# Performance work log

Measured on AMD Instinct MI355X. Metric: run time of the kernel, lower is better.

The kernel has to match this reference:

```python
import jax, jax.numpy as jnp
import numpy as np

H = 16      # num_heads
HD = 128    # head_dim = embed_dim // num_heads
BS = 64     # NSA block_size
SEL = 8     # selected blocks per query (block_counts)
WIN = 64    # sliding window (left) size
BASE = 10000.0


def _rope(t):
    # t: [b, n, h, hd]; rotary LRPE (lrpe_type=1)
    n, hd = t.shape[1], t.shape[-1]
    half = hd // 2
    inv = 1.0 / (BASE ** (jnp.arange(half, dtype=jnp.float32) / half))
    th = jnp.arange(n, dtype=jnp.float32)[:, None] * inv[None, :]  # [n, half]
    cos = jnp.cos(th)[None, :, None, :]
    sin = jnp.sin(th)[None, :, None, :]
    t1, t2 = t[..., :half], t[..., half:]
    return jnp.concatenate([t1 * cos - t2 * sin, t1 * sin + t2 * cos], axis=-1)


def _nsa_forward(x, Wq, Wk, Wv, Wg, Wo):
    b, n, d = x.shape
    nb = n // BS
    scale = HD ** -0.5
    q = (x @ Wq).reshape(b, n, H, HD)
    k = (x @ Wk).reshape(b, n, H, HD)
    v = (x @ Wv).reshape(b, n, H, HD)
    g = jax.nn.sigmoid(x @ Wg)                   # [b, n, 3H]
    g_cmp, g_slc, g_swa = jnp.split(g, 3, axis=-1)
    q = _rope(q)
    k = _rope(k)
    idx = jnp.arange(n)

    # --- compression branch: mean-pooled KV blocks, causal over fully-past blocks
    k_cmp = k.reshape(b, nb, BS, H, HD).mean(axis=2)   # [b, nb, h, hd]
    v_cmp = v.reshape(b, nb, BS, H, HD).mean(axis=2)
    s_cmp = jnp.einsum('bnhd,bmhd->bhnm', q, k_cmp) * scale  # [b, h, n, nb]
    blk_end = (jnp.arange(nb) + 1) * BS - 1
    cmp_mask = idx[:, None] >= blk_end[None, :]        # [n, nb]
    p_cmp = jax.nn.softmax(jnp.where(cmp_mask[None, None], s_cmp, -1e30), axis=-1)
    p_cmp = p_cmp * cmp_mask.any(-1)[None, None, :, None]  # zero rows with no valid block
    o_cmp = jnp.einsum('bhnm,bmhd->bnhd', p_cmp, v_cmp)

    # --- selection branch: top-k blocks by compressed scores, current block forced
    cur_blk = jax.nn.one_hot(idx // BS, nb, dtype=jnp.float32)  # [n, nb]
    imp = p_cmp + 2.0 * cur_blk[None, None]
    sel = jax.lax.top_k(imp, SEL)[1]                   # [b, h, n, SEL]
    blk_sel = jax.nn.one_hot(sel, nb).sum(-2) > 0      # [b, h, n, nb]
    causal = idx[:, None] >= idx[None, :]              # [n, n]
    slc_mask = blk_sel[..., idx // BS] & causal[None, None]  # [b, h, n, n]
    s_full = jnp.einsum('bnhd,bmhd->bhnm', q, k) * scale     # [b, h, n, n]
    p_slc = jax.nn.softmax(jnp.where(slc_mask, s_full, -1e30), axis=-1)
    o_slc = jnp.einsum('bhnm,bmhd->bnhd', p_slc, v)

    swa_mask = causal & (idx[:, None] - idx[None, :] <= WIN)
    p_swa = jax.nn.softmax(jnp.where(swa_mask[None, None], s_full, -1e30), axis=-1)
    o_swa = jnp.einsum('bhnm,bmhd->bnhd', p_swa, v)

    o = (o_cmp * g_cmp[..., None] + o_slc * g_slc[..., None]
         + o_swa * g_swa[..., None])                   # [b, n, h, hd]
    return o.reshape(b, n, H * HD) @ Wo


def setup_inputs() -> dict:
    key = jax.random.key(0)
    ks = jax.random.split(key, 6)
    B, N, D = 2, 1024, 2048
    std = 0.02
    return {
        'x': jax.random.normal(ks[0], (B, N, D), jnp.float32),
        'Wq': jax.random.normal(ks[1], (D, H * HD), jnp.float32) * std,
        'Wk': jax.random.normal(ks[2], (D, H * HD), jnp.float32) * std,
        'Wv': jax.random.normal(ks[3], (D, H * HD), jnp.float32) * std,
        'Wg': jax.random.normal(ks[4], (D, 3 * H), jnp.float32) * std,
        'Wo': jax.random.normal(ks[5], (H * HD, D), jnp.float32) * std,
    }


def reference(x, Wq, Wk, Wv, Wg, Wo):
    return _nsa_forward(x, Wq, Wk, Wv, Wg, Wo)
```

## Files before the change

kernel.cpp:

```cpp
#include <hip/hip_runtime.h>
#include <hip/hip_bf16.h>

#define HN   16
#define HDIM 128
#define NSEQ 1024
#define NBLK 16
#define BSZ  64
#define SCALE 0.08838834764831845f
#define QKV_STR 6400
#define KOFS 2048
#define VOFS 4096
#define GOFS 6144

typedef __attribute__((ext_vector_type(8))) short bfrag;
typedef __attribute__((ext_vector_type(4))) float facc;

__device__ __forceinline__ float bf2f(short s) {
  union { unsigned u; float f; } cv;
  cv.u = ((unsigned)(unsigned short)s) << 16;
  return cv.f;
}
__device__ __forceinline__ short f2bf(float f) {
  unsigned u = __float_as_uint(f);
  u = (u + 0x7fff + ((u >> 16) & 1)) >> 16;
  return (short)u;
}

#define ASYNC16(gp, lp)                                                    \
  __builtin_amdgcn_global_load_lds(                                        \
      (const __attribute__((address_space(1))) void*)(gp),                 \
      (__attribute__((address_space(3))) void*)(lp), 16, 0, 0)

#define MFMA16(a, b, c) __builtin_amdgcn_mfma_f32_16x16x32_bf16(a, b, c, 0, 0, 0)

__global__ __launch_bounds__(256) void prep(const float* __restrict__ Wq,
                                            const float* __restrict__ Wk,
                                            const float* __restrict__ Wv,
                                            const float* __restrict__ Wg,
                                            const float* __restrict__ x,
                                            short* __restrict__ w_t,
                                            short* __restrict__ x_bf,
                                            float2* __restrict__ tbl) {
  __shared__ float tile[32][33];
  const int z = blockIdx.z;
  const int bx = blockIdx.x * 32, by = blockIdx.y * 32;
  const int tx = threadIdx.x & 31, ty = threadIdx.x >> 5;
  if (z == 5) {
    if (blockIdx.y >= 4) return;
    int i = (blockIdx.y * 64 + blockIdx.x) * 256 + threadIdx.x;
    int d = i & 63, n = i >> 6;
    float inv = expf(-(float)d * (9.210340371976184f / 64.0f));
    float sn, cs;
    sincosf((float)n * inv, &sn, &cs);
    tbl[i] = make_float2(cs, sn);
    return;
  }
  if (z == 4) {
#pragma unroll
    for (int i = 0; i < 4; ++i) {
      const int row = by + ty + 8 * i;
      x_bf[(size_t)row * 2048 + bx + tx] = f2bf(x[(size_t)row * 2048 + bx + tx]);
    }
    return;
  }
  if (z == 3) {
    if (blockIdx.x >= 4) return;
#pragma unroll
    for (int i = 0; i < 4; ++i) {
      const int c = bx + tx;
      tile[ty + 8 * i][tx] = (c < 48) ? Wg[(size_t)(by + ty + 8 * i) * 48 + c] : 0.f;
    }
    __syncthreads();
#pragma unroll
    for (int i = 0; i < 4; ++i)
      w_t[(size_t)(GOFS + bx + ty + 8 * i) * 2048 + by + tx] = f2bf(tile[tx][ty + 8 * i]);
    return;
  }
  const float* src = (z == 0) ? Wq : (z == 1) ? Wk : Wv;
#pragma unroll
  for (int i = 0; i < 4; ++i)
    tile[ty + 8 * i][tx] = src[(size_t)(by + ty + 8 * i) * 2048 + bx + tx];
  __syncthreads();
#pragma unroll
  for (int i = 0; i < 4; ++i)
    w_t[(size_t)(z * 2048 + bx + ty + 8 * i) * 2048 + by + tx] = f2bf(tile[tx][ty + 8 * i]);
}

__global__ __launch_bounds__(256) void transpose_cast(const float* __restrict__ src,
                                                      short* __restrict__ dst) {
  __shared__ float tile[32][33];
  const int bx = blockIdx.x * 32, by = blockIdx.y * 32;
  const int tx = threadIdx.x & 31, ty = threadIdx.x >> 5;
#pragma unroll
  for (int i = 0; i < 4; ++i)
    tile[ty + 8 * i][tx] = src[(size_t)(by + ty + 8 * i) * 2048 + bx + tx];
  __syncthreads();
#pragma unroll
  for (int i = 0; i < 4; ++i)
    dst[(size_t)(bx + ty + 8 * i) * 2048 + by + tx] = f2bf(tile[tx][ty + 8 * i]);
}

__global__ __launch_bounds__(512, 1) void gemm256(const short* __restrict__ A,
                                                  const short* __restrict__ Bt,
                                                  short* __restrict__ C,
                                                  int M, int N, int K) {
  __shared__ short lds[2][2][16384];
  const int t = threadIdx.x;
  const int l = t & 63, w = t >> 6;
  const int wm = w >> 2, wn = w & 3;
  const int lm = l & 15, hi = l >> 4;
  const int lanexor = (lm & 7) << 3;
  const int kk0 = (hi * 8) ^ lanexor;
  const int L = blockIdx.x;
  const int item = (L & 7) * (gridDim.x >> 3) + (L >> 3);
  const int nrow = M >> 8;
  const int row0 = (item % nrow) * 256, col0 = (item / nrow) * 256;
  const int nt = K >> 6;

  const int srow = t >> 3;
  const int scol = 8 * ((t & 7) ^ (srow & 7));
  const short* Ab = A + (size_t)(row0 + srow) * K + scol;
  const short* Bb = Bt + (size_t)(col0 + srow) * K + scol;

#define STAGE(mat, srcbase, h, tau, buf)                                     \
  {                                                                          \
    const short* g_ = (srcbase) + (size_t)(h) * 128 * K + (size_t)(tau) * 64;\
    short* d_ = &lds[buf][mat][(h) * 8192 + t * 8];                          \
    ASYNC16(g_, d_);                                                         \
    ASYNC16(g_ + (size_t)64 * K, d_ + 4096);                                 \
  }

  facc acc[8][4] = {};
  bfrag af[8], bf0[4], bf1[4];

  STAGE(0, Ab, 0, 0, 0); STAGE(0, Ab, 1, 0, 0);
  STAGE(1, Bb, 0, 0, 0); STAGE(1, Bb, 1, 0, 0);
  STAGE(1, Bb, 0, 1, 1); STAGE(1, Bb, 1, 1, 1);
  asm volatile("s_waitcnt vmcnt(4)" ::: "memory");
  __builtin_amdgcn_s_barrier();

  for (int tau = 0; tau < nt; ++tau) {
    const int c = tau & 1;
    const int tA = (tau + 1 < nt) ? tau + 1 : nt - 1;
    const int tB = (tau + 2 < nt) ? tau + 2 : nt - 1;

#define DS_A(qm)                                                             \
  _Pragma("unroll") for (int ii = 0; ii < 4; ++ii) {                         \
    const int row_ = wm * 128 + (qm) * 64 + ii * 16 + lm;                    \
    af[ii * 2 + 0] = *(const bfrag*)&lds[c][0][row_ * 64 + kk0];             \
    af[ii * 2 + 1] = *(const bfrag*)&lds[c][0][row_ * 64 + (kk0 ^ 32)];      \
  }
#define DS_B(qn, arr)                                                        \
  _Pragma("unroll") for (int jj = 0; jj < 2; ++jj) {                         \
    const int row_ = wn * 64 + (qn) * 32 + jj * 16 + lm;                     \
    arr[jj * 2 + 0] = *(const bfrag*)&lds[c][1][row_ * 64 + kk0];            \
    arr[jj * 2 + 1] = *(const bfrag*)&lds[c][1][row_ * 64 + (kk0 ^ 32)];     \
  }
#define QUAD(qm, qn, arr)                                                    \
  _Pragma("unroll") for (int ii = 0; ii < 4; ++ii)                           \
  _Pragma("unroll") for (int jj = 0; jj < 2; ++jj) {                         \
    acc[(qm)*4+ii][(qn)*2+jj] = MFMA16(af[ii*2+0], arr[jj*2+0], acc[(qm)*4+ii][(qn)*2+jj]); \
    acc[(qm)*4+ii][(qn)*2+jj] = MFMA16(af[ii*2+1], arr[jj*2+1], acc[(qm)*4+ii][(qn)*2+jj]); \
  }

    DS_A(0); DS_B(0, bf0);
    STAGE(0, Ab, 0, tA, c ^ 1);
    __builtin_amdgcn_s_barrier();
    asm volatile("s_waitcnt lgkmcnt(0)" ::: "memory");
    __builtin_amdgcn_sched_barrier(0);
    __builtin_amdgcn_s_setprio(1);
    QUAD(0, 0, bf0);
    __builtin_amdgcn_s_setprio(0);
    __builtin_amdgcn_s_barrier();

    DS_B(1, bf1);
    STAGE(0, Ab, 1, tA, c ^ 1);
    __builtin_amdgcn_s_barrier();
    asm volatile("s_waitcnt lgkmcnt(0)" ::: "memory");
    __builtin_amdgcn_sched_barrier(0);
    __builtin_amdgcn_s_setprio(1);
    QUAD(0, 1, bf1);
    __builtin_amdgcn_s_setprio(0);
    __builtin_amdgcn_s_barrier();

    DS_A(1);
    STAGE(1, Bb, 0, tB, c);
    __builtin_amdgcn_s_barrier();
    asm volatile("s_waitcnt lgkmcnt(0)" ::: "memory");
    __builtin_amdgcn_sched_barrier(0);
    __builtin_amdgcn_s_setprio(1);
    QUAD(1, 1, bf1);
    __builtin_amdgcn_s_setprio(0);
    __builtin_amdgcn_s_barrier();

    STAGE(1, Bb, 1, tB, c);
    __builtin_amdgcn_s_setprio(1);
    QUAD(1, 0, bf0);
    __builtin_amdgcn_s_setprio(0);
    asm volatile("s_waitcnt vmcnt(4)" ::: "memory");
    __builtin_amdgcn_s_barrier();
  }

#pragma unroll
  for (int i = 0; i < 8; ++i)
#pragma unroll
    for (int j = 0; j < 4; ++j)
#pragma unroll
      for (int rr = 0; rr < 4; ++rr)
        C[(size_t)(row0 + wm * 128 + i * 16 + hi * 4 + rr) * N +
          col0 + wn * 64 + j * 16 + lm] = f2bf(acc[i][j][rr]);
#undef STAGE
#undef DS_A
#undef DS_B
#undef QUAD
}

__device__ __forceinline__ void store_c(float* p, float v) { *p = v; }
__device__ __forceinline__ void store_c(short* p, float v) { *p = f2bf(v); }

template <typename OT>
__global__ __launch_bounds__(256) void gemm_bf16_bt(const short* __restrict__ A,
                                                    const short* __restrict__ Bt,
                                                    OT* __restrict__ C,
                                                    int M, int N, int K) {
  __shared__ short As[128 * 32];
  __shared__ short Bs[128 * 32];
  const int t = threadIdx.x;
  const int l = t & 63, w = t >> 6;
  const int wr = w >> 1, wc = w & 1;
  const int nwg = gridDim.x;
  const int L = blockIdx.x;
  const int wg = (L & 7) * (nwg >> 3) + (L >> 3);
  const int nrow = M >> 7;
  const int row0 = (wg % nrow) * 128, col0 = (wg / nrow) * 128;
  facc acc[4][4] = {};

  const int sr = t >> 2;
  const int sk = (t & 3) * 8;
  const short* Ag0 = A + (size_t)(row0 + sr) * K + sk;
  const short* Ag1 = Ag0 + (size_t)64 * K;
  const short* Bg0 = Bt + (size_t)(col0 + sr) * K + sk;
  const short* Bg1 = Bg0 + (size_t)64 * K;
  short* la = As + t * 8;
  short* lb = Bs + t * 8;

  const int lm = l & 15;
  const int lk = (l >> 4) * 8;

  for (int k0 = 0; k0 < K; k0 += 32) {
    ASYNC16(Ag0 + k0, la);
    ASYNC16(Ag1 + k0, la + 2048);
    ASYNC16(Bg0 + k0, lb);
    ASYNC16(Bg1 + k0, lb + 2048);
    __syncthreads();
    bfrag af[4], bf[4];
#pragma unroll
    for (int i = 0; i < 4; ++i)
      af[i] = *(const bfrag*)&As[(wr * 64 + i * 16 + lm) * 32 + lk];
#pragma unroll
    for (int j = 0; j < 4; ++j)
      bf[j] = *(const bfrag*)&Bs[(wc * 64 + j * 16 + lm) * 32 + lk];
#pragma unroll
    for (int i = 0; i < 4; ++i)
#pragma unroll
      for (int j = 0; j < 4; ++j)
        acc[i][j] = MFMA16(af[i], bf[j], acc[i][j]);
    __syncthreads();
  }

  const int orow = row0 + wr * 64 + (l >> 4) * 4;
  const int ocol = col0 + wc * 64 + lm;
#pragma unroll
  for (int i = 0; i < 4; ++i)
#pragma unroll
    for (int j = 0; j < 4; ++j)
#pragma unroll
      for (int rr = 0; rr < 4; ++rr)
        store_c(&C[(size_t)(orow + i * 16 + rr) * N + ocol + j * 16], acc[i][j][rr]);
}

__global__ __launch_bounds__(256) void rope_qk(short* __restrict__ qkv,
                                               const float2* __restrict__ tbl) {
  int i = blockIdx.x * 256 + threadIdx.x;
  int c = i & 7;
  int h = (i >> 3) & 15;
  int qk = (i >> 7) & 1;
  int n = (i >> 8) & 1023;
  int b = i >> 18;
  short* base = qkv + (size_t)(b * NSEQ + n) * QKV_STR + qk * KOFS + h * HDIM + c * 8;
  const float2* tp = tbl + n * 64 + c * 8;
  bfrag t1 = *(const bfrag*)base, t2 = *(const bfrag*)(base + 64);
  bfrag o1, o2;
#pragma unroll
  for (int j = 0; j < 8; ++j) {
    float2 cssn = tp[j];
    float a = bf2f(t1[j]), bb = bf2f(t2[j]);
    o1[j] = f2bf(a * cssn.x - bb * cssn.y);
    o2[j] = f2bf(a * cssn.y + bb * cssn.x);
  }
  *(bfrag*)base = o1;
  *(bfrag*)(base + 64) = o2;
}

__global__ __launch_bounds__(256) void block_mean(const short* __restrict__ src,
                                                  float* __restrict__ dst) {
  int i = blockIdx.x * 256 + threadIdx.x;
  int d = i & 127;
  int h = (i >> 7) & 15;
  int m = (i >> 11) & 15;
  int b = i >> 15;
  const short* p = src + (size_t)(b * NSEQ + m * BSZ) * QKV_STR + h * HDIM + d;
  float acc = 0.f;
#pragma unroll 8
  for (int j = 0; j < 64; ++j) acc += bf2f(p[(size_t)j * QKV_STR]);
  dst[i] = acc * (1.0f / 64.0f);
}

__global__ __launch_bounds__(256) void v_transpose(const short* __restrict__ qkv,
                                                   short* __restrict__ vt,
                                                   short* __restrict__ vct) {
  __shared__ short tile[64][136];
  const int n0 = blockIdx.x * 64;
  const int h = blockIdx.y, b = blockIdx.z;
  const int t = threadIdx.x;
#pragma unroll
  for (int it = 0; it < 4; ++it) {
    int idx = t + 256 * it;
    int row = idx >> 4, ch = idx & 15;
    *(bfrag*)&tile[row][ch * 8] =
        *(const bfrag*)&qkv[(size_t)(b * NSEQ + n0 + row) * QKV_STR + VOFS + h * HDIM + ch * 8];
  }
  __syncthreads();
#pragma unroll
  for (int it = 0; it < 4; ++it) {
    int idx = t + 256 * it;
    int d = idx >> 3, ch = idx & 7;
    bfrag tv;
    float s = 0.f;
#pragma unroll
    for (int j = 0; j < 8; ++j) {
      tv[j] = tile[ch * 8 + j][d];
      s += bf2f(tv[j]);
    }
    *(bfrag*)&vt[(((size_t)(b * HN + h) * 128) + d) * 1024 + n0 + ch * 8] = tv;
    s += __shfl_down(s, 4);
    s += __shfl_down(s, 2);
    s += __shfl_down(s, 1);
    if ((t & 7) == 0)
      vct[(((size_t)(b * HN + h) * 128) + d) * 16 + (n0 >> 6)] = f2bf(s * (1.0f / 64.0f));
  }
}

__global__ __launch_bounds__(64) void cmp_sel(const short* __restrict__ qkv,
                                              const float* __restrict__ kc,
                                              short* __restrict__ pc,
                                              int* __restrict__ sel) {
  int i = blockIdx.x * 64 + threadIdx.x;
  int n = i & 1023;
  int h = (i >> 10) & 15;
  int b = i >> 14;
  const short* qp = qkv + (size_t)(b * NSEQ + n) * QKV_STR + h * HDIM;
  const int nv = (n + 1) >> 6;
  float s[NBLK];
#pragma unroll
  for (int m = 0; m < NBLK; ++m) s[m] = 0.f;
  for (int d0 = 0; d0 < HDIM; d0 += 8) {
    bfrag qv = *(const bfrag*)&qp[d0];
    float qf[8];
#pragma unroll
    for (int dd = 0; dd < 8; ++dd) qf[dd] = bf2f(qv[dd]);
    for (int m = 0; m < nv; ++m) {
      const float4* kp = (const float4*)(kc + ((size_t)((b * NBLK + m) * HN + h) << 7) + d0);
      const float4 k0 = kp[0], k1 = kp[1];
      s[m] += qf[0] * k0.x + qf[1] * k0.y + qf[2] * k0.z + qf[3] * k0.w +
              qf[4] * k1.x + qf[5] * k1.y + qf[6] * k1.z + qf[7] * k1.w;
    }
  }
  float mx = -1e30f;
  for (int m = 0; m < nv; ++m) { s[m] *= SCALE; mx = fmaxf(mx, s[m]); }
  float den = 0.f;
  for (int m = 0; m < nv; ++m) { s[m] = __expf(s[m] - mx); den += s[m]; }
  const float rden = (nv > 0) ? 1.0f / den : 0.f;
  float p[NBLK];
#pragma unroll
  for (int m = 0; m < NBLK; ++m) p[m] = (m < nv) ? s[m] * rden : 0.f;
  bfrag o0, o1;
#pragma unroll
  for (int m = 0; m < 8; ++m) { o0[m] = f2bf(p[m]); o1[m] = f2bf(p[m + 8]); }
  bfrag* pout = (bfrag*)(pc + (size_t)i * 16);
  pout[0] = o0; pout[1] = o1;
  p[n >> 6] += 2.0f;
  int mask = 0;
#pragma unroll
  for (int ss = 0; ss < 8; ++ss) {
    int best = 0;
    float bv = -1e30f;
#pragma unroll
    for (int m = 0; m < NBLK; ++m)
      if (p[m] > bv) { bv = p[m]; best = m; }
    mask |= 1 << best;
    p[best] = -1e30f;
  }
  sel[i] = mask;
}

__global__ __launch_bounds__(128, 2) void attn_mfma(
    const short* __restrict__ qkv, const short* __restrict__ vt,
    const short* __restrict__ vct, const short* __restrict__ pc,
    const int* __restrict__ sel, short* __restrict__ o) {
  const int fid = blockIdx.x;
  const int xcd = fid & 7;
  const int idx = fid >> 3;
  const int pair = (xcd << 2) | (idx & 3);
  const int rank = idx >> 2;
  const int h = pair & 15, b = pair >> 4;

  const int tid = threadIdx.x;
  const int wid = tid >> 6;
  const int rt = wid ? rank : 63 - rank;
  const int l = tid & 63;
  const int lm = l & 15, hi = l >> 4;
  const int nbase = rt * 16;

  __shared__ short pbuf[2][2][1024];
  short* p_slc = &pbuf[wid][0][0];
  short* p_swa = &pbuf[wid][1][0];

  const short* qrow = qkv + (size_t)(b * NSEQ + nbase + lm) * QKV_STR + h * HDIM;
  bfrag qf[4];
#pragma unroll
  for (int ks = 0; ks < 4; ++ks) qf[ks] = *(const bfrag*)&qrow[32 * ks + 8 * hi];

  int selrow = sel[(size_t)(b * HN + h) * NSEQ + nbase + lm];
  int uni = selrow;
#pragma unroll
  for (int m = 1; m < 16; m <<= 1) uni |= __shfl_xor(uni, m);
  int sel4[4];
#pragma unroll
  for (int rg = 0; rg < 4; ++rg) sel4[rg] = __shfl(selrow, 4 * hi + rg);

  const int thi = nbase >> 6;
  const int tlo = (nbase >= 64) ? ((nbase - 64) >> 6) : 0;
  const int wmask = (int)((2u << thi) - (1u << tlo));
  const unsigned am = (unsigned)(uni | wmask) & (unsigned)((2u << thi) - 1);

  facc acc_slc[8] = {}, acc_swa[8] = {};
  float ps_s[4] = {0.f, 0.f, 0.f, 0.f}, ps_w[4] = {0.f, 0.f, 0.f, 0.f};

  const short* kbase0 = qkv + (size_t)(b * NSEQ) * QKV_STR + KOFS + h * HDIM + 8 * hi;
  const short* vtb0 = vt + ((size_t)(b * HN + h) * 128) * 1024 + 8 * hi;

#define LOADK4(d0, d1, d2, d3, colbase)                                     \
  {                                                                         \
    const short* kr_ = kbase0 + (size_t)((colbase) + lm) * QKV_STR;         \
    d0 = *(const bfrag*)(kr_);                                              \
    d1 = *(const bfrag*)(kr_ + 32);                                         \
    d2 = *(const bfrag*)(kr_ + 64);                                         \
    d3 = *(const bfrag*)(kr_ + 96);                                         \
  }

#define MFMA4(dst, s0, s1, s2, s3)                                          \
  dst = MFMA16(qf[0], s0, dst);                                             \
  dst = MFMA16(qf[1], s1, dst);                                             \
  dst = MFMA16(qf[2], s2, dst);                                             \
  dst = MFMA16(qf[3], s3, dst);

#define EXPF(f_)                                                            \
  _Pragma("unroll") for (int rg = 0; rg < 4; ++rg) {                        \
    const int col_ = ct * 64 + 16 * (f_) + lm;                              \
    const int row_ = nbase + 4 * hi + rg;                                   \
    float e_ = __expf(sacc[f_][rg] * SCALE);                                \
    e_ = (col_ <= row_) ? e_ : 0.f;                                         \
    float es_ = ((sel4[rg] >> ct) & 1) ? e_ : 0.f;                          \
    float ew_ = (row_ - col_ <= 64) ? e_ : 0.f;                             \
    ps_s[rg] += es_;                                                        \
    ps_w[rg] += ew_;                                                        \
    const int srow_ = 4 * hi + rg;                                          \
    const int sidx_ = (64 * srow_ + 16 * (f_) + lm) ^ ((srow_ & 7) << 3);   \
    if (do_s) p_slc[sidx_] = f2bf(es_);                                     \
    if (do_w) p_swa[sidx_] = f2bf(ew_);                                     \
  }

  int ct = __ffs((int)am) - 1;
  bfrag ka0, ka1, ka2, ka3;
  LOADK4(ka0, ka1, ka2, ka3, ct * 64);

  while (ct >= 0) {
    const unsigned rem = am & ~((2u << ct) - 1);
    const int nct = rem ? (__ffs((int)rem) - 1) : -1;
    const bool do_s = (uni >> ct) & 1;
    const bool do_w = (wmask >> ct) & 1;
    const short* vtb = vtb0 + ct * 64;

    facc sacc[4] = {};
    bfrag kb0, kb1, kb2, kb3, kc0, kc1, kc2, kc3, kd0, kd1, kd2, kd3;
    bfrag vb0[8], vb1[8];

    LOADK4(kb0, kb1, kb2, kb3, ct * 64 + 16);
    MFMA4(sacc[0], ka0, ka1, ka2, ka3);

    LOADK4(kc0, kc1, kc2, kc3, ct * 64 + 32);
#pragma unroll
    for (int df = 0; df < 8; ++df)
      vb0[df] = *(const bfrag*)&vtb[(size_t)(16 * df + lm) * 1024];
    EXPF(0);
    MFMA4(sacc[1], kb0, kb1, kb2, kb3);

    LOADK4(kd0, kd1, kd2, kd3, ct * 64 + 48);
#pragma unroll
    for (int df = 0; df < 8; ++df)
      vb1[df] = *(const bfrag*)&vtb[(size_t)(16 * df + lm) * 1024 + 32];
    EXPF(1);
    MFMA4(sacc[2], kc0, kc1, kc2, kc3);

    LOADK4(ka0, ka1, ka2, ka3, (nct >= 0 ? nct : ct) * 64);
    EXPF(2);
    MFMA4(sacc[3], kd0, kd1, kd2, kd3);
    EXPF(3);

    {
      const int ridx0 = (64 * lm + 8 * hi) ^ ((lm & 7) << 3);
      bfrag pas = {}, paw = {};
      if (do_s) pas = *(const bfrag*)&p_slc[ridx0];
      if (do_w) paw = *(const bfrag*)&p_swa[ridx0];
#pragma unroll
      for (int df = 0; df < 8; ++df) {
        if (do_s) acc_slc[df] = MFMA16(pas, vb0[df], acc_slc[df]);
        if (do_w) acc_swa[df] = MFMA16(paw, vb0[df], acc_swa[df]);
      }
      const int ridx1 = (64 * lm + 8 * hi + 32) ^ ((lm & 7) << 3);
      bfrag pas1 = {}, paw1 = {};
      if (do_s) pas1 = *(const bfrag*)&p_slc[ridx1];
      if (do_w) paw1 = *(const bfrag*)&p_swa[ridx1];
#pragma unroll
      for (int df = 0; df < 8; ++df) {
        if (do_s) acc_slc[df] = MFMA16(pas1, vb1[df], acc_slc[df]);
        if (do_w) acc_swa[df] = MFMA16(paw1, vb1[df], acc_swa[df]);
      }
    }
    ct = nct;
  }
#undef LOADK4
#undef MFMA4
#undef EXPF

  facc acc_cmp[8] = {};
  {
    bfrag pa = {};
    if (hi < 2)
      pa = *(const bfrag*)&pc[((size_t)(b * HN + h) * NSEQ + nbase + lm) * 16 + 8 * hi];
#pragma unroll
    for (int df = 0; df < 8; ++df) {
      bfrag vb = {};
      if (hi < 2)
        vb = *(const bfrag*)&vct[(((size_t)(b * HN + h) * 128) + 16 * df + lm) * 16 + 8 * hi];
      acc_cmp[df] = MFMA16(pa, vb, acc_cmp[df]);
    }
  }

#pragma unroll
  for (int m = 1; m < 16; m <<= 1) {
#pragma unroll
    for (int rg = 0; rg < 4; ++rg) {
      ps_s[rg] += __shfl_xor(ps_s[rg], m);
      ps_w[rg] += __shfl_xor(ps_w[rg], m);
    }
  }

  float inv_s[4], inv_w[4], gcv[4], gsv[4], gwv[4];
#pragma unroll
  for (int rg = 0; rg < 4; ++rg) {
    inv_s[rg] = 1.0f / ps_s[rg];
    inv_w[rg] = 1.0f / ps_w[rg];
    const short* gp = qkv + (size_t)(b * NSEQ + nbase + 4 * hi + rg) * QKV_STR + GOFS;
    gcv[rg] = 1.0f / (1.0f + __expf(-bf2f(gp[h])));
    gsv[rg] = 1.0f / (1.0f + __expf(-bf2f(gp[16 + h])));
    gwv[rg] = 1.0f / (1.0f + __expf(-bf2f(gp[32 + h])));
  }

  short* obase = o + (size_t)(b * NSEQ + nbase) * 2048 + h * HDIM;
#pragma unroll
  for (int df = 0; df < 8; ++df)
#pragma unroll
    for (int rg = 0; rg < 4; ++rg) {
      float val = gcv[rg] * acc_cmp[df][rg] +
                  gsv[rg] * acc_slc[df][rg] * inv_s[rg] +
                  gwv[rg] * acc_swa[df][rg] * inv_w[rg];
      obase[(size_t)(4 * hi + rg) * 2048 + 16 * df + lm] = f2bf(val);
    }
}

extern "C" void kernel_launch(void* const* d_in, const int* in_sizes, int n_in,
                              void* d_out, int out_size, void* d_ws, size_t ws_size,
                              hipStream_t stream) {
  const float* x  = (const float*)d_in[0];
  const float* Wq = (const float*)d_in[1];
  const float* Wk = (const float*)d_in[2];
  const float* Wv = (const float*)d_in[3];
  const float* Wg = (const float*)d_in[4];
  const float* Wo = (const float*)d_in[5];
  float* out = (float*)d_out;

  char* w = (char*)d_ws;
  short* x_bf = (short*)w;
  short* o_bf = x_bf;
  w += (size_t)2048 * 2048 * 2;
  short* w_t  = (short*)w;
  w += (size_t)6400 * 2048 * 2;
  short* qkv  = (short*)w;
  w += (size_t)2048 * 6400 * 2;
  float* kc   = (float*)w; w += (size_t)65536 * 4;
  short* vct  = (short*)w; w += (size_t)65536 * 2;
  short* pcb  = (short*)w; w += (size_t)524288 * 2;
  int*   sel  = (int*)w;   w += (size_t)32768 * 4;
  short* vt   = (short*)w; w += (size_t)4194304 * 2;
  float2* tbl = (float2*)w; w += (size_t)65536 * 8;

  const dim3 blk(256);
  prep<<<dim3(64, 64, 6), blk, 0, stream>>>(Wq, Wk, Wv, Wg, x, w_t, x_bf, tbl);
  gemm256<<<200, dim3(512), 0, stream>>>(x_bf, w_t, qkv, 2048, 6400, 2048);
  rope_qk<<<2048, blk, 0, stream>>>(qkv, tbl);
  block_mean<<<256, blk, 0, stream>>>(qkv + KOFS, kc);
  v_transpose<<<dim3(16, 16, 2), blk, 0, stream>>>(qkv, vt, vct);
  cmp_sel<<<512, dim3(64), 0, stream>>>(qkv, kc, pcb, sel);
  transpose_cast<<<dim3(64, 64), blk, 0, stream>>>(Wo, w_t);
  attn_mfma<<<1024, dim3(128), 0, stream>>>(qkv, vt, vct, pcb, sel, o_bf);
  gemm_bf16_bt<float><<<256, blk, 0, stream>>>(o_bf, w_t, out, 2048, 2048, 2048);
}
```

Before: 260.9 us.

## Share double-buffered K/V tiles in LDS across eight waves in attention

The attention kernel moves from 128-thread blocks, where each wave loaded K and V^T straight from global memory, to 512-thread blocks of eight waves. The waves cover interleaved 16-row query tiles of one (batch, head) and share each 64-column K/V tile. Tiles are copied into swizzled LDS with async copies and double buffering, so each K/V tile is fetched once per block rather than once per wave. In exchange it adds a block-wide barrier per column tile and walks every tile up to the block's maximum, skipping compute where a wave's mask bit is clear. It also raises LDS use, which lowers occupancy.

After: 242.1 us. 7.2% less time.

```diff
diff --git a/kernel.cpp b/kernel.cpp
--- a/kernel.cpp
+++ b/kernel.cpp
@@ -404,7 +404,7 @@
   sel[i] = mask;
 }
 
-__global__ __launch_bounds__(128, 2) void attn_mfma(
+__global__ __launch_bounds__(512, 1) void attn_mfma(
     const short* __restrict__ qkv, const short* __restrict__ vt,
     const short* __restrict__ vct, const short* __restrict__ pc,
     const int* __restrict__ sel, short* __restrict__ o) {
@@ -412,17 +412,20 @@
   const int xcd = fid & 7;
   const int idx = fid >> 3;
   const int pair = (xcd << 2) | (idx & 3);
-  const int rank = idx >> 2;
+  const int rblk = idx >> 2;
   const int h = pair & 15, b = pair >> 4;
 
   const int tid = threadIdx.x;
   const int wid = tid >> 6;
-  const int rt = wid ? rank : 63 - rank;
   const int l = tid & 63;
   const int lm = l & 15, hi = l >> 4;
+  const int rt = wid * 8 + rblk;
   const int nbase = rt * 16;
-
-  __shared__ short pbuf[2][2][1024];
+  const int CTMAX = ((56 + rblk) * 16) >> 6;
+
+  __shared__ short kbuf[2][8192];
+  __shared__ short vbuf[2][8192];
+  __shared__ short pbuf[8][2][1024];
   short* p_slc = &pbuf[wid][0][0];
   short* p_swa = &pbuf[wid][1][0];
 
@@ -447,23 +450,23 @@
   facc acc_slc[8] = {}, acc_swa[8] = {};
   float ps_s[4] = {0.f, 0.f, 0.f, 0.f}, ps_w[4] = {0.f, 0.f, 0.f, 0.f};
 
-  const short* kbase0 = qkv + (size_t)(b * NSEQ) * QKV_STR + KOFS + h * HDIM + 8 * hi;
-  const short* vtb0 = vt + ((size_t)(b * HN + h) * 128) * 1024 + 8 * hi;
-
-#define LOADK4(d0, d1, d2, d3, colbase)                                     \
-  {                                                                         \
-    const short* kr_ = kbase0 + (size_t)((colbase) + lm) * QKV_STR;         \
-    d0 = *(const bfrag*)(kr_);                                              \
-    d1 = *(const bfrag*)(kr_ + 32);                                         \
-    d2 = *(const bfrag*)(kr_ + 64);                                         \
-    d3 = *(const bfrag*)(kr_ + 96);                                         \
-  }
-
-#define MFMA4(dst, s0, s1, s2, s3)                                          \
-  dst = MFMA16(qf[0], s0, dst);                                             \
-  dst = MFMA16(qf[1], s1, dst);                                             \
-  dst = MFMA16(qf[2], s2, dst);                                             \
-  dst = MFMA16(qf[3], s3, dst);
+#define STAGEKV(ct_, buf_)                                                   \
+  {                                                                          \
+    _Pragma("unroll") for (int rr = 0; rr < 2; ++rr) {                       \
+      const int i2 = tid + 512 * rr;                                         \
+      const int rw = i2 >> 4, cc = i2 & 15;                                  \
+      const short* g_ = qkv + (size_t)(b * NSEQ + (ct_) * 64 + rw) * QKV_STR \
+                        + KOFS + h * HDIM + 8 * (cc ^ (rw & 7));             \
+      ASYNC16(g_, &kbuf[buf_][i2 * 8]);                                      \
+    }                                                                        \
+    _Pragma("unroll") for (int rr = 0; rr < 2; ++rr) {                       \
+      const int i2 = tid + 512 * rr;                                         \
+      const int dd = i2 >> 3, cc = i2 & 7;                                   \
+      const short* g_ = vt + ((size_t)(b * HN + h) * 128 + dd) * 1024        \
+                        + (ct_) * 64 + 8 * (cc ^ (dd & 7));                  \
+      ASYNC16(g_, &vbuf[buf_][i2 * 8]);                                      \
+    }                                                                        \
+  }
 
 #define EXPF(f_)                                                            \
   _Pragma("unroll") for (int rg = 0; rg < 4; ++rg) {                        \
@@ -481,67 +484,55 @@
     if (do_w) p_swa[sidx_] = f2bf(ew_);                                     \
   }
 
-  int ct = __ffs((int)am) - 1;
-  bfrag ka0, ka1, ka2, ka3;
-  LOADK4(ka0, ka1, ka2, ka3, ct * 64);
-
-  while (ct >= 0) {
-    const unsigned rem = am & ~((2u << ct) - 1);
-    const int nct = rem ? (__ffs((int)rem) - 1) : -1;
-    const bool do_s = (uni >> ct) & 1;
-    const bool do_w = (wmask >> ct) & 1;
-    const short* vtb = vtb0 + ct * 64;
-
-    facc sacc[4] = {};
-    bfrag kb0, kb1, kb2, kb3, kc0, kc1, kc2, kc3, kd0, kd1, kd2, kd3;
-    bfrag vb0[8], vb1[8];
-
-    LOADK4(kb0, kb1, kb2, kb3, ct * 64 + 16);
-    MFMA4(sacc[0], ka0, ka1, ka2, ka3);
-
-    LOADK4(kc0, kc1, kc2, kc3, ct * 64 + 32);
-#pragma unroll
-    for (int df = 0; df < 8; ++df)
-      vb0[df] = *(const bfrag*)&vtb[(size_t)(16 * df + lm) * 1024];
-    EXPF(0);
-    MFMA4(sacc[1], kb0, kb1, kb2, kb3);
-
-    LOADK4(kd0, kd1, kd2, kd3, ct * 64 + 48);
-#pragma unroll
-    for (int df = 0; df < 8; ++df)
-      vb1[df] = *(const bfrag*)&vtb[(size_t)(16 * df + lm) * 1024 + 32];
-    EXPF(1);
-    MFMA4(sacc[2], kc0, kc1, kc2, kc3);
-
-    LOADK4(ka0, ka1, ka2, ka3, (nct >= 0 ? nct : ct) * 64);
-    EXPF(2);
-    MFMA4(sacc[3], kd0, kd1, kd2, kd3);
-    EXPF(3);
-
-    {
-      const int ridx0 = (64 * lm + 8 * hi) ^ ((lm & 7) << 3);
-      bfrag pas = {}, paw = {};
-      if (do_s) pas = *(const bfrag*)&p_slc[ridx0];
-      if (do_w) paw = *(const bfrag*)&p_swa[ridx0];
-#pragma unroll
-      for (int df = 0; df < 8; ++df) {
-        if (do_s) acc_slc[df] = MFMA16(pas, vb0[df], acc_slc[df]);
-        if (do_w) acc_swa[df] = MFMA16(paw, vb0[df], acc_swa[df]);
+  STAGEKV(0, 0);
+  asm volatile("s_waitcnt vmcnt(0)" ::: "memory");
+  __syncthreads();
+
+  for (int ct = 0; ct <= CTMAX; ++ct) {
+    const int cur = ct & 1;
+    if (ct < CTMAX) STAGEKV(ct + 1, cur ^ 1);
+
+    if ((am >> ct) & 1) {
+      const bool do_s = (uni >> ct) & 1;
+      const bool do_w = (wmask >> ct) & 1;
+
+      facc sacc[4] = {};
+#pragma unroll
+      for (int f = 0; f < 4; ++f) {
+        const int row_ = 16 * f + lm;
+        const int rx = row_ & 7;
+        bfrag k0 = *(const bfrag*)&kbuf[cur][row_ * 128 + 8 * ((0 + hi) ^ rx)];
+        bfrag k1 = *(const bfrag*)&kbuf[cur][row_ * 128 + 8 * ((4 + hi) ^ rx)];
+        bfrag k2 = *(const bfrag*)&kbuf[cur][row_ * 128 + 8 * ((8 + hi) ^ rx)];
+        bfrag k3 = *(const bfrag*)&kbuf[cur][row_ * 128 + 8 * ((12 + hi) ^ rx)];
+        sacc[f] = MFMA16(qf[0], k0, sacc[f]);
+        sacc[f] = MFMA16(qf[1], k1, sacc[f]);
+        sacc[f] = MFMA16(qf[2], k2, sacc[f]);
+        sacc[f] = MFMA16(qf[3], k3, sacc[f]);
       }
-      const int ridx1 = (64 * lm + 8 * hi + 32) ^ ((lm & 7) << 3);
-      bfrag pas1 = {}, paw1 = {};
-      if (do_s) pas1 = *(const bfrag*)&p_slc[ridx1];
-      if (do_w) paw1 = *(const bfrag*)&p_swa[ridx1];
-#pragma unroll
-      for (int df = 0; df < 8; ++df) {
-        if (do_s) acc_slc[df] = MFMA16(pas1, vb1[df], acc_slc[df]);
-        if (do_w) acc_swa[df] = MFMA16(paw1, vb1[df], acc_swa[df]);
+
+      EXPF(0); EXPF(1); EXPF(2); EXPF(3);
+
+#pragma unroll
+      for (int ks = 0; ks < 2; ++ks) {
+        const int ridx = (64 * lm + 8 * hi + 32 * ks) ^ ((lm & 7) << 3);
+        bfrag pas = {}, paw = {};
+        if (do_s) pas = *(const bfrag*)&p_slc[ridx];
+        if (do_w) paw = *(const bfrag*)&p_swa[ridx];
+#pragma unroll
+        for (int df = 0; df < 8; ++df) {
+          const int d_ = 16 * df + lm;
+          bfrag vb = *(const bfrag*)&vbuf[cur][d_ * 64 + 8 * ((4 * ks + hi) ^ (d_ & 7))];
+          if (do_s) acc_slc[df] = MFMA16(pas, vb, acc_slc[df]);
+          if (do_w) acc_swa[df] = MFMA16(paw, vb, acc_swa[df]);
+        }
       }
     }
-    ct = nct;
-  }
-#undef LOADK4
-#undef MFMA4
+
+    asm volatile("s_waitcnt vmcnt(0)" ::: "memory");
+    __syncthreads();
+  }
+#undef STAGEKV
 #undef EXPF
 
   facc acc_cmp[8] = {};
@@ -624,6 +615,6 @@
   v_transpose<<<dim3(16, 16, 2), blk, 0, stream>>>(qkv, vt, vct);
   cmp_sel<<<512, dim3(64), 0, stream>>>(qkv, kc, pcb, sel);
   transpose_cast<<<dim3(64, 64), blk, 0, stream>>>(Wo, w_t);
-  attn_mfma<<<1024, dim3(128), 0, stream>>>(qkv, vt, vct, pcb, sel, o_bf);
+  attn_mfma<<<256, dim3(512), 0, stream>>>(qkv, vt, vct, pcb, sel, o_bf);
   gemm_bf16_bt<float><<<256, blk, 0, stream>>>(o_bf, w_t, out, 2048, 2048, 2048);
 }
```
